# Kernel tuning notes

Hardware: AMD Instinct MI355X
Metric: run time of the kernel (lower is better)

## Reference

```python
import jax, jax.numpy as jnp
import numpy as np

K = 1000   # grid rows (detections from model 1, truncated to 1000)
N = 1000   # grid cols (detections from model 2)
M = 900000 # number of non-empty (overlapping) pairs
F = 7      # per-pair feature dim
SENTINEL = -9999.0


def setup_inputs() -> dict:
    key = jax.random.key(0)
    ks = jax.random.split(key, 12)
    def w(k, o, i):
        return jax.random.normal(k, (o, i), dtype=jnp.float32) * 0.05
    def b(k, o):
        return jax.random.normal(k, (o,), dtype=jnp.float32) * 0.05
    return {
        "input_1": jax.random.normal(ks[0], (1, F, 1, M), dtype=jnp.float32),
        "T_out": jnp.zeros((1, K, N), dtype=jnp.float32),
        "T_indices": jax.random.randint(ks[1], (2, M), 0, K),
        "w1": w(ks[2], 18, F),  "b1": b(ks[3], 18),
        "w2": w(ks[4], 36, 18), "b2": b(ks[5], 36),
        "w3": w(ks[6], 36, 36), "b3": b(ks[7], 36),
        "w4": w(ks[8], 1, 36),  "b4": b(ks[9], 1),
    }


def reference(input_1, T_out, T_indices, w1, b1, w2, b2, w3, b3, w4, b4):
    # 1x1 conv stack == channel matmuls on the flattened [F, M] features.
    x = input_1[0, :, 0, :]                       # [F, M]
    h = jax.nn.relu(w1 @ x + b1[:, None])         # [18, M]
    h = jax.nn.relu(w2 @ h + b2[:, None])         # [36, M]
    h = jax.nn.relu(w3 @ h + b3[:, None])         # [36, M]
    vals = (w4 @ h + b4[:, None])[0]              # [M]

    grid = jnp.full(T_out.shape, SENTINEL, dtype=T_out.dtype)  # [1, K, N]
    grid = grid.at[:, T_indices[0], T_indices[1]].set(vals[None, :])

    # MaxPool2d([1, N]) -> max over cols; MaxPool2d([K, 1]) -> max over rows.
    row_max = grid.max(axis=2).squeeze()          # [K]
    col_max = grid.max(axis=1).squeeze()          # [N]
    return (row_max, col_max)
```

## Files before the change

kernel.cpp:

```cpp
#include <hip/hip_runtime.h>
#include <stdint.h>

#define KK 1000
#define NN 1000
#define MM 900000
#define FF 7
#define SENTINEL -9999.0f

template <int N, typename F>
__device__ __forceinline__ void unroll_loop(F&& f) {
    if constexpr (N > 0) {
        unroll_loop<N - 1>(static_cast<F&&>(f));
        f(N - 1);
    }
}

__global__ __launch_bounds__(256) void init_grid(ulonglong2* __restrict__ g, int n2) {
    int i = blockIdx.x * 256 + threadIdx.x;
    if (i < n2) g[i] = make_ulonglong2(0ULL, 0ULL);
}

__global__ __launch_bounds__(256, 4) void mlp_scatter(
    const float* __restrict__ in,
    const int*   __restrict__ idx,
    const float* __restrict__ w1, const float* __restrict__ b1,
    const float* __restrict__ w2, const float* __restrict__ b2,
    const float* __restrict__ w3, const float* __restrict__ b3,
    const float* __restrict__ w4, const float* __restrict__ b4,
    unsigned long long* __restrict__ grid)
{
    int m = blockIdx.x * 256 + threadIdx.x;
    if (m >= MM) return;

    float x[FF];
    unroll_loop<FF>([&](int f) { x[f] = in[f * MM + m]; });

    float h1[18];
    unroll_loop<18>([&](int o) {
        float a = b1[o];
        unroll_loop<FF>([&](int i) { a = fmaf(w1[o * FF + i], x[i], a); });
        h1[o] = fmaxf(a, 0.0f);
    });

    float h2[36];
    unroll_loop<36>([&](int o) {
        float a = b2[o];
        unroll_loop<18>([&](int i) { a = fmaf(w2[o * 18 + i], h1[i], a); });
        h2[o] = fmaxf(a, 0.0f);
    });

    float v = b4[0];
    unroll_loop<36>([&](int o) {
        float a = b3[o];
        unroll_loop<36>([&](int i) { a = fmaf(w3[o * 36 + i], h2[i], a); });
        v = fmaf(w4[o], fmaxf(a, 0.0f), v);
    });

    int r = idx[m];
    int c = idx[MM + m];
    unsigned long long packed =
        ((unsigned long long)(unsigned)(m + 1) << 32) | (unsigned)__float_as_uint(v);
    atomicMax(&grid[r * NN + c], packed);
}

__global__ __launch_bounds__(256) void row_max_k(const unsigned long long* __restrict__ g,
                                                 float* __restrict__ out) {
    int r = blockIdx.x;
    float mx = SENTINEL;
    for (int c = threadIdx.x; c < NN; c += 256) {
        unsigned long long p = g[(size_t)r * NN + c];
        if (p) mx = fmaxf(mx, __uint_as_float((unsigned)p));
    }
    __shared__ float red[256];
    red[threadIdx.x] = mx;
    __syncthreads();
    for (int s = 128; s > 0; s >>= 1) {
        if (threadIdx.x < s) red[threadIdx.x] = fmaxf(red[threadIdx.x], red[threadIdx.x + s]);
        __syncthreads();
    }
    if (threadIdx.x == 0) out[r] = red[0];
}

#define CCHUNKS 25
#define CROWS   (KK / CCHUNKS)

__global__ __launch_bounds__(256) void col_partial(const unsigned long long* __restrict__ g,
                                                   float* __restrict__ part) {
    int n = blockIdx.x * 256 + threadIdx.x;
    if (n >= NN) return;
    int k0 = blockIdx.y * CROWS;
    float mx = SENTINEL;
    for (int k = k0; k < k0 + CROWS; ++k) {
        unsigned long long p = g[(size_t)k * NN + n];
        if (p) mx = fmaxf(mx, __uint_as_float((unsigned)p));
    }
    part[blockIdx.y * NN + n] = mx;
}

__global__ __launch_bounds__(256) void col_final(const float* __restrict__ part,
                                                 float* __restrict__ out) {
    int n = blockIdx.x * 256 + threadIdx.x;
    if (n >= NN) return;
    float mx = SENTINEL;
#pragma unroll
    for (int c = 0; c < CCHUNKS; ++c) mx = fmaxf(mx, part[c * NN + n]);
    out[KK + n] = mx;
}

extern "C" void kernel_launch(void* const* d_in, const int* in_sizes, int n_in,
                              void* d_out, int out_size, void* d_ws, size_t ws_size,
                              hipStream_t stream) {
    const float* in  = (const float*)d_in[0];
    const int*   idx = (const int*)d_in[2];
    const float* w1  = (const float*)d_in[3];
    const float* b1  = (const float*)d_in[4];
    const float* w2  = (const float*)d_in[5];
    const float* b2  = (const float*)d_in[6];
    const float* w3  = (const float*)d_in[7];
    const float* b3  = (const float*)d_in[8];
    const float* w4  = (const float*)d_in[9];
    const float* b4  = (const float*)d_in[10];

    unsigned long long* grid = (unsigned long long*)d_ws;
    float* part = (float*)((char*)d_ws + (size_t)KK * NN * 8);
    float* out  = (float*)d_out;

    const int n2 = (KK * NN) / 2;
    init_grid<<<(n2 + 255) / 256, 256, 0, stream>>>((ulonglong2*)grid, n2);

    mlp_scatter<<<(MM + 255) / 256, 256, 0, stream>>>(
        in, idx, w1, b1, w2, b2, w3, b3, w4, b4, grid);

    row_max_k<<<KK, 256, 0, stream>>>(grid, out);
    col_partial<<<dim3(4, CCHUNKS), 256, 0, stream>>>(grid, part);
    col_final<<<4, 256, 0, stream>>>(part, out);
}
```

Measured before the change: 171.9 us.

## Stage MLP weights in LDS, process two pairs per thread, shuffle row reduction

Each block now copies all MLP weights and biases into shared memory once, and each thread evaluates the MLP for two pairs (m and m+HALF), so every weight load feeds two FMAs. The launch bound drops to 2 blocks per SM so the doubled register state fits. The row-max reduction switches from a shared-memory tree to wavefront shuffles. The aim is to cut per-FMA weight-load overhead and reduction sync cost, at the risk of lower occupancy and register spilling. Out-of-range threads are clamped to the last index and write duplicate atomics, which is harmless because the packed values are identical.

```diff
diff --git a/kernel.cpp b/kernel.cpp
--- a/kernel.cpp
+++ b/kernel.cpp
@@ -4,23 +4,31 @@
 #define KK 1000
 #define NN 1000
 #define MM 900000
+#define HALF 450000
 #define FF 7
 #define SENTINEL -9999.0f
 
-template <int N, typename F>
-__device__ __forceinline__ void unroll_loop(F&& f) {
-    if constexpr (N > 0) {
-        unroll_loop<N - 1>(static_cast<F&&>(f));
-        f(N - 1);
-    }
-}
+#define R18(X) X(0) X(1) X(2) X(3) X(4) X(5) X(6) X(7) X(8) X(9) X(10) X(11) \
+               X(12) X(13) X(14) X(15) X(16) X(17)
+#define R36(X) R18(X) X(18) X(19) X(20) X(21) X(22) X(23) X(24) X(25) X(26) \
+               X(27) X(28) X(29) X(30) X(31) X(32) X(33) X(34) X(35)
+
+#define OW1 0
+#define OB1 126
+#define OW2 144
+#define OB2 792
+#define OW3 828
+#define OB3 2124
+#define OW4 2160
+#define OB4 2196
+#define WTOT 2197
 
 __global__ __launch_bounds__(256) void init_grid(ulonglong2* __restrict__ g, int n2) {
     int i = blockIdx.x * 256 + threadIdx.x;
     if (i < n2) g[i] = make_ulonglong2(0ULL, 0ULL);
 }
 
-__global__ __launch_bounds__(256, 4) void mlp_scatter(
+__global__ __launch_bounds__(256, 2) void mlp_scatter(
     const float* __restrict__ in,
     const int*   __restrict__ idx,
     const float* __restrict__ w1, const float* __restrict__ b1,
@@ -29,38 +37,75 @@
     const float* __restrict__ w4, const float* __restrict__ b4,
     unsigned long long* __restrict__ grid)
 {
-    int m = blockIdx.x * 256 + threadIdx.x;
-    if (m >= MM) return;
+    __shared__ float W[WTOT];
+    int tid = threadIdx.x;
+    for (int i = tid; i < 126;  i += 256) W[OW1 + i] = w1[i];
+    for (int i = tid; i < 18;   i += 256) W[OB1 + i] = b1[i];
+    for (int i = tid; i < 648;  i += 256) W[OW2 + i] = w2[i];
+    for (int i = tid; i < 36;   i += 256) W[OB2 + i] = b2[i];
+    for (int i = tid; i < 1296; i += 256) W[OW3 + i] = w3[i];
+    for (int i = tid; i < 36;   i += 256) W[OB3 + i] = b3[i];
+    for (int i = tid; i < 36;   i += 256) W[OW4 + i] = w4[i];
+    if (tid == 0) W[OB4] = b4[0];
+    __syncthreads();
 
-    float x[FF];
-    unroll_loop<FF>([&](int f) { x[f] = in[f * MM + m]; });
+    int t = blockIdx.x * 256 + tid;
+    if (t >= HALF) t = HALF - 1;
+    int mA = t, mB = t + HALF;
 
-    float h1[18];
-    unroll_loop<18>([&](int o) {
-        float a = b1[o];
-        unroll_loop<FF>([&](int i) { a = fmaf(w1[o * FF + i], x[i], a); });
-        h1[o] = fmaxf(a, 0.0f);
-    });
+    float x0_0 = in[0*MM+mA], x0_1 = in[0*MM+mB];
+    float x1_0 = in[1*MM+mA], x1_1 = in[1*MM+mB];
+    float x2_0 = in[2*MM+mA], x2_1 = in[2*MM+mB];
+    float x3_0 = in[3*MM+mA], x3_1 = in[3*MM+mB];
+    float x4_0 = in[4*MM+mA], x4_1 = in[4*MM+mB];
+    float x5_0 = in[5*MM+mA], x5_1 = in[5*MM+mB];
+    float x6_0 = in[6*MM+mA], x6_1 = in[6*MM+mB];
 
-    float h2[36];
-    unroll_loop<36>([&](int o) {
-        float a = b2[o];
-        unroll_loop<18>([&](int i) { a = fmaf(w2[o * 18 + i], h1[i], a); });
-        h2[o] = fmaxf(a, 0.0f);
-    });
+#define L1(o) float h1_##o##_0, h1_##o##_1; { \
+    float a0 = W[OB1+(o)], a1 = a0, w; \
+    w=W[OW1+(o)*7+0]; a0=fmaf(w,x0_0,a0); a1=fmaf(w,x0_1,a1); \
+    w=W[OW1+(o)*7+1]; a0=fmaf(w,x1_0,a0); a1=fmaf(w,x1_1,a1); \
+    w=W[OW1+(o)*7+2]; a0=fmaf(w,x2_0,a0); a1=fmaf(w,x2_1,a1); \
+    w=W[OW1+(o)*7+3]; a0=fmaf(w,x3_0,a0); a1=fmaf(w,x3_1,a1); \
+    w=W[OW1+(o)*7+4]; a0=fmaf(w,x4_0,a0); a1=fmaf(w,x4_1,a1); \
+    w=W[OW1+(o)*7+5]; a0=fmaf(w,x5_0,a0); a1=fmaf(w,x5_1,a1); \
+    w=W[OW1+(o)*7+6]; a0=fmaf(w,x6_0,a0); a1=fmaf(w,x6_1,a1); \
+    h1_##o##_0=fmaxf(a0,0.0f); h1_##o##_1=fmaxf(a1,0.0f); }
+    R18(L1)
+#undef L1
 
-    float v = b4[0];
-    unroll_loop<36>([&](int o) {
-        float a = b3[o];
-        unroll_loop<36>([&](int i) { a = fmaf(w3[o * 36 + i], h2[i], a); });
-        v = fmaf(w4[o], fmaxf(a, 0.0f), v);
-    });
+#define T2(o,i) w=W[OW2+(o)*18+(i)]; a0=fmaf(w,h1_##i##_0,a0); a1=fmaf(w,h1_##i##_1,a1);
+#define L2(o) float h2_##o##_0, h2_##o##_1; { \
+    float a0 = W[OB2+(o)], a1 = a0, w; \
+    T2(o,0) T2(o,1) T2(o,2) T2(o,3) T2(o,4) T2(o,5) T2(o,6) T2(o,7) T2(o,8) \
+    T2(o,9) T2(o,10) T2(o,11) T2(o,12) T2(o,13) T2(o,14) T2(o,15) T2(o,16) T2(o,17) \
+    h2_##o##_0=fmaxf(a0,0.0f); h2_##o##_1=fmaxf(a1,0.0f); }
+    R36(L2)
+#undef L2
+#undef T2
 
-    int r = idx[m];
-    int c = idx[MM + m];
-    unsigned long long packed =
-        ((unsigned long long)(unsigned)(m + 1) << 32) | (unsigned)__float_as_uint(v);
-    atomicMax(&grid[r * NN + c], packed);
+    float v0 = W[OB4], v1 = v0;
+#define T3(o,i) w=W[OW3+(o)*36+(i)]; a0=fmaf(w,h2_##i##_0,a0); a1=fmaf(w,h2_##i##_1,a1);
+#define L34(o) { float a0 = W[OB3+(o)], a1 = a0, w; \
+    T3(o,0)  T3(o,1)  T3(o,2)  T3(o,3)  T3(o,4)  T3(o,5)  T3(o,6)  T3(o,7)  \
+    T3(o,8)  T3(o,9)  T3(o,10) T3(o,11) T3(o,12) T3(o,13) T3(o,14) T3(o,15) \
+    T3(o,16) T3(o,17) T3(o,18) T3(o,19) T3(o,20) T3(o,21) T3(o,22) T3(o,23) \
+    T3(o,24) T3(o,25) T3(o,26) T3(o,27) T3(o,28) T3(o,29) T3(o,30) T3(o,31) \
+    T3(o,32) T3(o,33) T3(o,34) T3(o,35) \
+    w = W[OW4+(o)]; \
+    v0 = fmaf(w, fmaxf(a0,0.0f), v0); v1 = fmaf(w, fmaxf(a1,0.0f), v1); }
+    R36(L34)
+#undef L34
+#undef T3
+
+    int rA = idx[mA], cA = idx[MM + mA];
+    int rB = idx[mB], cB = idx[MM + mB];
+    unsigned long long pA =
+        ((unsigned long long)(unsigned)(mA + 1) << 32) | (unsigned)__float_as_uint(v0);
+    unsigned long long pB =
+        ((unsigned long long)(unsigned)(mB + 1) << 32) | (unsigned)__float_as_uint(v1);
+    atomicMax(&grid[rA * NN + cA], pA);
+    atomicMax(&grid[rB * NN + cB], pB);
 }
 
 __global__ __launch_bounds__(256) void row_max_k(const unsigned long long* __restrict__ g,
@@ -71,14 +116,11 @@
         unsigned long long p = g[(size_t)r * NN + c];
         if (p) mx = fmaxf(mx, __uint_as_float((unsigned)p));
     }
-    __shared__ float red[256];
-    red[threadIdx.x] = mx;
+    for (int s = 32; s > 0; s >>= 1) mx = fmaxf(mx, __shfl_down(mx, s, 64));
+    __shared__ float red[4];
+    if ((threadIdx.x & 63) == 0) red[threadIdx.x >> 6] = mx;
     __syncthreads();
-    for (int s = 128; s > 0; s >>= 1) {
-        if (threadIdx.x < s) red[threadIdx.x] = fmaxf(red[threadIdx.x], red[threadIdx.x + s]);
-        __syncthreads();
-    }
-    if (threadIdx.x == 0) out[r] = red[0];
+    if (threadIdx.x == 0) out[r] = fmaxf(fmaxf(red[0], red[1]), fmaxf(red[2], red[3]));
 }
 
 #define CCHUNKS 25
@@ -128,7 +170,7 @@
     const int n2 = (KK * NN) / 2;
     init_grid<<<(n2 + 255) / 256, 256, 0, stream>>>((ulonglong2*)grid, n2);
 
-    mlp_scatter<<<(MM + 255) / 256, 256, 0, stream>>>(
+    mlp_scatter<<<(HALF + 255) / 256, 256, 0, stream>>>(
         in, idx, w1, b1, w2, b2, w3, b3, w4, b4, grid);
 
     row_max_k<<<KK, 256, 0, stream>>>(grid, out);
```

Measured after the change: 175.3 us. Within noise of the previous version (+2.0%).
